# Optimization experiments

Hardware: AMD Instinct MI355X
Metric: run time of the kernel (lower is better)

## Reference

```python
import jax, jax.numpy as jnp
import numpy as np

B, T, V, C, NB, NOPS = 8, 2048, 4096, 128, 64, 8

_NONLIN = [
    lambda h: h,
    jax.nn.relu,
    lambda h: jax.nn.gelu(h, approximate=False),
    lambda h: jnp.square(h),
    lambda h: -h,
    jnp.abs,
    jnp.tanh,
    jax.nn.sigmoid,
]


def setup_inputs() -> dict:
    key = jax.random.key(0)
    ks = jax.random.split(key, 6)
    s = 0.02
    return {
        "x": jax.random.normal(ks[0], (B, T, V), dtype=jnp.float32),
        "basis": jax.random.normal(ks[1], (V, 2 * NB), dtype=jnp.float32),
        "read_coeffs": jax.random.normal(ks[2], (C, 2 * NB), dtype=jnp.float32) * s,
        "write_coeffs": jax.random.normal(ks[3], (C, 2 * NB), dtype=jnp.float32) * s,
        "op_logits": jnp.zeros((NOPS,), dtype=jnp.float32),
        "op_weights": jax.random.normal(ks[4], (NOPS, C, C), dtype=jnp.float32) * s,
        "op_biases": jnp.zeros((NOPS, C), dtype=jnp.float32),
        "out_scale": jnp.float32(0.1),
    }


def op_bank(values, op_logits, op_weights, op_biases):
    # values: (B, T, C); soft mixture of 8 small channel transforms
    w = jax.nn.softmax(op_logits)  # (n_ops,)
    result = jnp.zeros_like(values)
    for i in range(NOPS):
        h = values @ op_weights[i] + op_biases[i]
        h = _NONLIN[i % len(_NONLIN)](h)
        result = result + w[i] * h
    return result


def reference(x, basis, read_coeffs, write_coeffs, op_logits, op_weights, op_biases, out_scale):
    # READ: Fourier soft addressing over V registers, normalized over registers (axis 0)
    read_w = jax.nn.softmax(basis @ read_coeffs.T, axis=0)  # (V, C)
    values = x @ read_w  # (B, T, C)
    # SELECT OP + APPLY
    values = op_bank(values, op_logits, op_weights, op_biases)
    # WRITE: unnormalized Fourier addressing back to registers
    write_w = basis @ write_coeffs.T  # (V, C)
    return (values @ write_w.T) * out_scale  # (B, T, V)
```

## Files before the change

kernel.cpp:

```cpp
#include <hip/hip_runtime.h>
#include <math.h>

#define M_TOT 16384
#define V_DIM 4096
#define C_DIM 128

typedef __bf16 bf16;
typedef __bf16 bf16x8 __attribute__((ext_vector_type(8)));
typedef float f32x4 __attribute__((ext_vector_type(4)));

__device__ inline f32x4 zero4() { f32x4 z; z[0]=0.f; z[1]=0.f; z[2]=0.f; z[3]=0.f; return z; }

__device__ inline bf16 f2bf(float f) {
  union { float f; unsigned u; } a; a.f = f;
  unsigned r = (a.u + 0x7FFFu + ((a.u >> 16) & 1u)) >> 16;
  union { unsigned short s; bf16 b; } o; o.s = (unsigned short)r;
  return o.b;
}

__device__ inline bf16x8 cvt8(float4 a, float4 b) {
  bf16x8 r;
  r[0]=f2bf(a.x); r[1]=f2bf(a.y); r[2]=f2bf(a.z); r[3]=f2bf(a.w);
  r[4]=f2bf(b.x); r[5]=f2bf(b.y); r[6]=f2bf(b.z); r[7]=f2bf(b.w);
  return r;
}

__device__ inline void gld_lds16(const void* g, void* l) {
  __builtin_amdgcn_global_load_lds((const __attribute__((address_space(1))) void*)g,
                                   (__attribute__((address_space(3))) void*)l, 16, 0, 0);
}

union PrepU {
  struct { bf16 A[128][136]; bf16 B[128][136]; } lg;
  struct { bf16 A[64][136];  bf16 B[128][136]; } w2;
};

__global__ __launch_bounds__(256) void k_prep(const float* __restrict__ basis,
                                              const float* __restrict__ rc,
                                              const float* __restrict__ wc,
                                              const float* __restrict__ opw,
                                              float* __restrict__ LT,
                                              bf16* __restrict__ W2,
                                              bf16* __restrict__ WTO) {
  __shared__ __align__(16) PrepU pu;
  const int t = threadIdx.x;
  const int bid = blockIdx.x;
  const int lane = t & 63, wave = t >> 6, fm = lane & 15, quad = lane >> 4;

  if (bid < 32) {
    const int v0 = bid * 128;
    {
      const int row = t >> 1, c0 = (t & 1) * 64;
      const float4* p = (const float4*)(rc + row * 128 + c0);
      bf16x8* d = (bf16x8*)&pu.lg.A[row][c0];
#pragma unroll
      for (int j = 0; j < 8; j++) { float4 a = p[2*j], b = p[2*j+1]; d[j] = cvt8(a, b); }
    }
    {
      const int row = t >> 1, c0 = (t & 1) * 64;
      const float4* p = (const float4*)(basis + (size_t)(v0 + row) * 128 + c0);
      bf16x8* d = (bf16x8*)&pu.lg.B[row][c0];
#pragma unroll
      for (int j = 0; j < 8; j++) { float4 a = p[2*j], b = p[2*j+1]; d[j] = cvt8(a, b); }
    }
    __syncthreads();

    f32x4 acc[2][8];
#pragma unroll
    for (int m = 0; m < 2; m++)
#pragma unroll
      for (int n = 0; n < 8; n++) acc[m][n] = zero4();

#pragma unroll
    for (int kk = 0; kk < 4; kk++) {
      bf16x8 af[2];
#pragma unroll
      for (int m = 0; m < 2; m++)
        af[m] = *(const bf16x8*)&pu.lg.A[wave * 32 + m * 16 + fm][kk * 32 + quad * 8];
#pragma unroll
      for (int nt = 0; nt < 8; nt++) {
        bf16x8 bfr = *(const bf16x8*)&pu.lg.B[nt * 16 + fm][kk * 32 + quad * 8];
#pragma unroll
        for (int m = 0; m < 2; m++)
          acc[m][nt] = __builtin_amdgcn_mfma_f32_16x16x32_bf16(af[m], bfr, acc[m][nt], 0, 0, 0);
      }
    }
#pragma unroll
    for (int m = 0; m < 2; m++)
#pragma unroll
      for (int nt = 0; nt < 8; nt++)
#pragma unroll
        for (int r = 0; r < 4; r++) {
          int c = wave * 32 + m * 16 + quad * 4 + r;
          LT[(size_t)c * V_DIM + v0 + nt * 16 + fm] = acc[m][nt][r];
        }
  } else if (bid < 96) {
    const int v0 = (bid - 32) * 64;
    {
      const int row = t >> 2, c0 = (t & 3) * 32;
      const float4* p = (const float4*)(basis + (size_t)(v0 + row) * 128 + c0);
      bf16x8* d = (bf16x8*)&pu.w2.A[row][c0];
#pragma unroll
      for (int j = 0; j < 4; j++) { float4 a = p[2*j], b = p[2*j+1]; d[j] = cvt8(a, b); }
    }
    {
      const int row = t >> 1, c0 = (t & 1) * 64;
      const float4* p = (const float4*)(wc + row * 128 + c0);
      bf16x8* d = (bf16x8*)&pu.w2.B[row][c0];
#pragma unroll
      for (int j = 0; j < 8; j++) { float4 a = p[2*j], b = p[2*j+1]; d[j] = cvt8(a, b); }
    }
    __syncthreads();

    f32x4 acc[8];
#pragma unroll
    for (int n = 0; n < 8; n++) acc[n] = zero4();
#pragma unroll
    for (int kk = 0; kk < 4; kk++) {
      bf16x8 af = *(const bf16x8*)&pu.w2.A[wave * 16 + fm][kk * 32 + quad * 8];
#pragma unroll
      for (int nt = 0; nt < 8; nt++) {
        bf16x8 bfr = *(const bf16x8*)&pu.w2.B[nt * 16 + fm][kk * 32 + quad * 8];
        acc[nt] = __builtin_amdgcn_mfma_f32_16x16x32_bf16(af, bfr, acc[nt], 0, 0, 0);
      }
    }
#pragma unroll
    for (int nt = 0; nt < 8; nt++)
#pragma unroll
      for (int r = 0; r < 4; r++) {
        int v = v0 + wave * 16 + quad * 4 + r;
        W2[v * 128 + nt * 16 + fm] = f2bf(acc[nt][r]);
      }
  } else {
    int idx = (bid - 96) * 256 + t;
    int i = idx >> 14, rem = idx & 16383, n = rem >> 7, k = rem & 127;
    WTO[idx] = f2bf(opw[(i << 14) + k * 128 + n]);
  }
}

__global__ __launch_bounds__(256) void k_softmax(const float* __restrict__ LT,
                                                 bf16* __restrict__ RT) {
  const int c = blockIdx.x, t = threadIdx.x;
  __shared__ float red[256];
  const float* row = LT + (size_t)c * V_DIM;
  float e[16];
  float lmax = -3.0e38f;
#pragma unroll
  for (int j = 0; j < 16; j++) { e[j] = row[t + 256 * j]; lmax = fmaxf(lmax, e[j]); }
  red[t] = lmax;
  __syncthreads();
  for (int off = 128; off > 0; off >>= 1) {
    if (t < off) red[t] = fmaxf(red[t], red[t + off]);
    __syncthreads();
  }
  const float gmax = red[0];
  __syncthreads();
  float lsum = 0.f;
#pragma unroll
  for (int j = 0; j < 16; j++) { e[j] = __expf(e[j] - gmax); lsum += e[j]; }
  red[t] = lsum;
  __syncthreads();
  for (int off = 128; off > 0; off >>= 1) {
    if (t < off) red[t] += red[t + off];
    __syncthreads();
  }
  const float inv = 1.f / red[0];
#pragma unroll
  for (int j = 0; j < 16; j++)
    RT[(size_t)c * V_DIM + t + 256 * j] = f2bf(e[j] * inv);
}

__global__ __launch_bounds__(256, 4) void k_gemm1(const float* __restrict__ x,
                                                  const bf16* __restrict__ RT,
                                                  bf16* __restrict__ PART) {
  __shared__ __align__(16) bf16 Bsm[2][128][64];
  const int t = threadIdx.x;
  const int kc = blockIdx.x & 3;
  const int m0 = (blockIdx.x >> 2) * 64;
  const int lane = t & 63, wave = t >> 6;
  const int fm = lane & 15, quad = lane >> 4;
  const int sw = (fm & 7) << 4;

  const int c_row = wave * 32 + (lane >> 3);
  const int src_colbyte = ((lane & 7) * 16) ^ ((lane >> 3) << 4);
  const bf16* bp = RT + (size_t)c_row * V_DIM + (src_colbyte >> 1);

  const float* xp = x + (size_t)(m0 + wave * 16 + fm) * V_DIM + quad * 8;

  f32x4 acc[8];
#pragma unroll
  for (int i = 0; i < 8; i++) acc[i] = zero4();

  const int kbeg = kc * 1024;

#define G1_ISSUE_B(buf, koff)                                                  \
  {                                                                            \
    _Pragma("unroll")                                                          \
    for (int jj = 0; jj < 4; jj++)                                             \
      gld_lds16(bp + (size_t)jj * 8 * V_DIM + (koff),                          \
                (char*)&Bsm[buf][0][0] + (wave * 4 + jj) * 1024);              \
  }

#define G1_ISSUE_A(p0, p1, p2, p3, koff)                                       \
  {                                                                            \
    p0 = *(const float4*)(xp + (koff));                                        \
    p1 = *(const float4*)(xp + (koff) + 4);                                    \
    p2 = *(const float4*)(xp + (koff) + 32);                                   \
    p3 = *(const float4*)(xp + (koff) + 36);                                   \
  }

#define G1_COMPUTE(buf, p0, p1, p2, p3)                                        \
  {                                                                            \
    bf16x8 af0 = cvt8(p0, p1);                                                 \
    bf16x8 af1 = cvt8(p2, p3);                                                 \
    const char* bb = (const char*)&Bsm[buf][0][0];                             \
    _Pragma("unroll")                                                          \
    for (int nt = 0; nt < 8; nt++) {                                           \
      const char* rp = bb + (nt * 16 + fm) * 128;                              \
      bf16x8 b0 = *(const bf16x8*)(rp + ((quad * 16) ^ sw));                   \
      bf16x8 b1 = *(const bf16x8*)(rp + ((64 + quad * 16) ^ sw));              \
      acc[nt] = __builtin_amdgcn_mfma_f32_16x16x32_bf16(af0, b0, acc[nt], 0, 0, 0); \
      acc[nt] = __builtin_amdgcn_mfma_f32_16x16x32_bf16(af1, b1, acc[nt], 0, 0, 0); \
    }                                                                          \
  }

  float4 aE0, aE1, aE2, aE3, aO0, aO1, aO2, aO3;

  G1_ISSUE_B(0, kbeg);
  G1_ISSUE_A(aE0, aE1, aE2, aE3, kbeg);

#pragma unroll
  for (int s = 0; s < 8; s++) {
    const int k0 = kbeg + s * 128;
    __syncthreads();
    G1_ISSUE_B(1, k0 + 64);
    G1_ISSUE_A(aO0, aO1, aO2, aO3, k0 + 64);
    G1_COMPUTE(0, aE0, aE1, aE2, aE3);
    __syncthreads();
    if (s < 7) {
      G1_ISSUE_B(0, k0 + 128);
      G1_ISSUE_A(aE0, aE1, aE2, aE3, k0 + 128);
    }
    G1_COMPUTE(1, aO0, aO1, aO2, aO3);
  }
#undef G1_ISSUE_B
#undef G1_ISSUE_A
#undef G1_COMPUTE

  bf16* po = PART + (size_t)kc * (M_TOT * C_DIM);
#pragma unroll
  for (int nt = 0; nt < 8; nt++)
#pragma unroll
    for (int r = 0; r < 4; r++) {
      int row = m0 + wave * 16 + quad * 4 + r;
      po[row * 128 + nt * 16 + fm] = f2bf(acc[nt][r]);
    }
}

__device__ inline float apply_nonlin(int i, float v) {
  switch (i) {
    case 0: return v;
    case 1: return fmaxf(v, 0.f);
    case 2: return 0.5f * v * (1.f + erff(v * 0.70710678118654752f));
    case 3: return v * v;
    case 4: return -v;
    case 5: return fabsf(v);
    case 6: return tanhf(v);
    default: return 1.f / (1.f + __expf(-v));
  }
}

__global__ __launch_bounds__(256) void k_opbank(const bf16* __restrict__ PART,
                                                const bf16* __restrict__ WTO,
                                                const float* __restrict__ op_logits,
                                                const float* __restrict__ op_biases,
                                                bf16* __restrict__ val2) {
  __shared__ __align__(16) bf16 Asm[32][136];
  __shared__ __align__(16) bf16 Bsm[128][136];
  const int t = threadIdx.x;
  const int m0 = blockIdx.x * 32;
  const int lane = t & 63, wave = t >> 6;
  const int fm = lane & 15, quad = lane >> 4;
  const int mf = wave & 1, nh = wave >> 1;

  float w[8];
  {
    float lm = -3.0e38f;
#pragma unroll
    for (int i = 0; i < 8; i++) { w[i] = op_logits[i]; lm = fmaxf(lm, w[i]); }
    float s = 0.f;
#pragma unroll
    for (int i = 0; i < 8; i++) { w[i] = __expf(w[i] - lm); s += w[i]; }
    float inv = 1.f / s;
#pragma unroll
    for (int i = 0; i < 8; i++) w[i] *= inv;
  }

  {
    const int row = t >> 3, c0 = (t & 7) * 16;
    float accA[16];
#pragma unroll
    for (int j = 0; j < 16; j++) accA[j] = 0.f;
#pragma unroll
    for (int p = 0; p < 4; p++) {
      const bf16x8* q = (const bf16x8*)(PART + (size_t)p * (M_TOT * C_DIM) + (m0 + row) * 128 + c0);
      bf16x8 u0 = q[0], u1 = q[1];
#pragma unroll
      for (int j = 0; j < 8; j++) { accA[j] += (float)u0[j]; accA[8 + j] += (float)u1[j]; }
    }
    bf16x8 o0, o1;
#pragma unroll
    for (int j = 0; j < 8; j++) { o0[j] = f2bf(accA[j]); o1[j] = f2bf(accA[8 + j]); }
    *(bf16x8*)&Asm[row][c0] = o0;
    *(bf16x8*)&Asm[row][c0 + 8] = o1;
  }
  __syncthreads();

  bf16x8 af[4];
#pragma unroll
  for (int kk = 0; kk < 4; kk++)
    af[kk] = *(const bf16x8*)&Asm[mf * 16 + fm][kk * 32 + quad * 8];

  f32x4 res[4];
#pragma unroll
  for (int j = 0; j < 4; j++) res[j] = zero4();

  const int brow = t >> 1, boff = (t & 1) * 64;
  for (int i = 0; i < 8; i++) {
    __syncthreads();
    {
      const uint4* p = (const uint4*)(WTO + i * 16384 + brow * 128 + boff);
      uint4* d = (uint4*)&Bsm[brow][boff];
#pragma unroll
      for (int j = 0; j < 8; j++) d[j] = p[j];
    }
    __syncthreads();
#pragma unroll
    for (int j = 0; j < 4; j++) {
      const int nt = nh * 4 + j;
      f32x4 h = zero4();
#pragma unroll
      for (int kk = 0; kk < 4; kk++) {
        bf16x8 bfr = *(const bf16x8*)&Bsm[nt * 16 + fm][kk * 32 + quad * 8];
        h = __builtin_amdgcn_mfma_f32_16x16x32_bf16(af[kk], bfr, h, 0, 0, 0);
      }
      float bias = op_biases[i * 128 + nt * 16 + fm];
#pragma unroll
      for (int r = 0; r < 4; r++) {
        float vv = h[r] + bias;
        res[j][r] += w[i] * apply_nonlin(i, vv);
      }
    }
  }
#pragma unroll
  for (int j = 0; j < 4; j++) {
    const int nt = nh * 4 + j;
#pragma unroll
    for (int r = 0; r < 4; r++) {
      int row = m0 + mf * 16 + quad * 4 + r;
      val2[row * 128 + nt * 16 + fm] = f2bf(res[j][r]);
    }
  }
}

struct G2S { bf16 A[64][136]; bf16 B[128][136]; };
union G2U { G2S s; float C[64][132]; };

__global__ __launch_bounds__(256) void k_gemm2(const bf16* __restrict__ val2,
                                               const bf16* __restrict__ W2,
                                               const float* __restrict__ p_scale,
                                               float* __restrict__ out) {
  __shared__ __align__(16) G2U u;
  const int t = threadIdx.x;
  const int n0 = (blockIdx.x >> 8) * 128;
  const int m0 = (blockIdx.x & 255) * 64;
  const int lane = t & 63, wave = t >> 6;
  const int fm = lane & 15, quad = lane >> 4;

  {
    const int row = t >> 2, off = (t & 3) * 32;
    const uint4* p = (const uint4*)(val2 + (m0 + row) * 128 + off);
    uint4* d = (uint4*)&u.s.A[row][off];
#pragma unroll
    for (int j = 0; j < 4; j++) d[j] = p[j];
  }
  {
    const int row = t >> 1, off = (t & 1) * 64;
    const uint4* p = (const uint4*)(W2 + (n0 + row) * 128 + off);
    uint4* d = (uint4*)&u.s.B[row][off];
#pragma unroll
    for (int j = 0; j < 8; j++) d[j] = p[j];
  }
  __syncthreads();

  const float scale = *p_scale;
  bf16x8 af[4];
#pragma unroll
  for (int kk = 0; kk < 4; kk++)
    af[kk] = *(const bf16x8*)&u.s.A[wave * 16 + fm][kk * 32 + quad * 8];

  f32x4 acc[8];
#pragma unroll
  for (int nt = 0; nt < 8; nt++) {
    acc[nt] = zero4();
#pragma unroll
    for (int kk = 0; kk < 4; kk++) {
      bf16x8 bfr = *(const bf16x8*)&u.s.B[nt * 16 + fm][kk * 32 + quad * 8];
      acc[nt] = __builtin_amdgcn_mfma_f32_16x16x32_bf16(af[kk], bfr, acc[nt], 0, 0, 0);
    }
  }
  __syncthreads();
#pragma unroll
  for (int nt = 0; nt < 8; nt++)
#pragma unroll
    for (int r = 0; r < 4; r++)
      u.C[wave * 16 + quad * 4 + r][nt * 16 + fm] = acc[nt][r] * scale;
  __syncthreads();
#pragma unroll
  for (int j = 0; j < 8; j++) {
    int idx = t + 256 * j;
    int row = idx >> 5, c4 = idx & 31;
    float4 v = *(const float4*)&u.C[row][c4 * 4];
    *(float4*)(out + (size_t)(m0 + row) * V_DIM + n0 + c4 * 4) = v;
  }
}

extern "C" void kernel_launch(void* const* d_in, const int* in_sizes, int n_in,
                              void* d_out, int out_size, void* d_ws, size_t ws_size,
                              hipStream_t stream) {
  const float* x      = (const float*)d_in[0];
  const float* basis  = (const float*)d_in[1];
  const float* rc     = (const float*)d_in[2];
  const float* wc     = (const float*)d_in[3];
  const float* oplog  = (const float*)d_in[4];
  const float* opw    = (const float*)d_in[5];
  const float* opb    = (const float*)d_in[6];
  const float* oscale = (const float*)d_in[7];
  float* out = (float*)d_out;
  char* ws = (char*)d_ws;

  float* LT  = (float*)(ws);
  bf16* RT   = (bf16*)(ws + 2097152);
  bf16* W2   = (bf16*)(ws + 3145728);
  bf16* WTO  = (bf16*)(ws + 4194304);
  bf16* PART = (bf16*)(ws + 4456448);
  bf16* VAL2 = (bf16*)(ws + 21233664);

  k_prep   <<<608, 256, 0, stream>>>(basis, rc, wc, opw, LT, W2, WTO);
  k_softmax<<<C_DIM, 256, 0, stream>>>(LT, RT);
  k_gemm1  <<<(M_TOT / 64) * 4, 256, 0, stream>>>(x, RT, PART);
  k_opbank <<<M_TOT / 32, 256, 0, stream>>>(PART, WTO, oplog, opb, VAL2);
  k_gemm2  <<<(M_TOT / 64) * (V_DIM / 128), 256, 0, stream>>>(VAL2, W2, oscale, out);
}
```

Baseline: 577.3 us.

## Fuse read GEMM, op bank and write GEMM into one per-tile kernel

Replaces the split-K read GEMM, the op-bank kernel and the write GEMM with a single kernel. Each block handles 64 rows: it runs the full K=4096 reduction, then applies the eight op transforms from shared memory, then streams the output in 32 column tiles with W2 tiles prefetched through registers. The goal is to drop the partial-sum and intermediate buffers and their global round trips, plus two launches. The cost is a grid of only 256 blocks of 256 threads, so latency hiding is much weaker, and output stores now go straight from MFMA fragments instead of being staged for coalescing.

New measurement: 644.7 us. 11.7% more time.

```diff
diff --git a/kernel.cpp b/kernel.cpp
--- a/kernel.cpp
+++ b/kernel.cpp
@@ -170,93 +170,6 @@
     RT[(size_t)c * V_DIM + t + 256 * j] = f2bf(e[j] * inv);
 }
 
-__global__ __launch_bounds__(256, 4) void k_gemm1(const float* __restrict__ x,
-                                                  const bf16* __restrict__ RT,
-                                                  bf16* __restrict__ PART) {
-  __shared__ __align__(16) bf16 Bsm[2][128][64];
-  const int t = threadIdx.x;
-  const int kc = blockIdx.x & 3;
-  const int m0 = (blockIdx.x >> 2) * 64;
-  const int lane = t & 63, wave = t >> 6;
-  const int fm = lane & 15, quad = lane >> 4;
-  const int sw = (fm & 7) << 4;
-
-  const int c_row = wave * 32 + (lane >> 3);
-  const int src_colbyte = ((lane & 7) * 16) ^ ((lane >> 3) << 4);
-  const bf16* bp = RT + (size_t)c_row * V_DIM + (src_colbyte >> 1);
-
-  const float* xp = x + (size_t)(m0 + wave * 16 + fm) * V_DIM + quad * 8;
-
-  f32x4 acc[8];
-#pragma unroll
-  for (int i = 0; i < 8; i++) acc[i] = zero4();
-
-  const int kbeg = kc * 1024;
-
-#define G1_ISSUE_B(buf, koff)                                                  \
-  {                                                                            \
-    _Pragma("unroll")                                                          \
-    for (int jj = 0; jj < 4; jj++)                                             \
-      gld_lds16(bp + (size_t)jj * 8 * V_DIM + (koff),                          \
-                (char*)&Bsm[buf][0][0] + (wave * 4 + jj) * 1024);              \
-  }
-
-#define G1_ISSUE_A(p0, p1, p2, p3, koff)                                       \
-  {                                                                            \
-    p0 = *(const float4*)(xp + (koff));                                        \
-    p1 = *(const float4*)(xp + (koff) + 4);                                    \
-    p2 = *(const float4*)(xp + (koff) + 32);                                   \
-    p3 = *(const float4*)(xp + (koff) + 36);                                   \
-  }
-
-#define G1_COMPUTE(buf, p0, p1, p2, p3)                                        \
-  {                                                                            \
-    bf16x8 af0 = cvt8(p0, p1);                                                 \
-    bf16x8 af1 = cvt8(p2, p3);                                                 \
-    const char* bb = (const char*)&Bsm[buf][0][0];                             \
-    _Pragma("unroll")                                                          \
-    for (int nt = 0; nt < 8; nt++) {                                           \
-      const char* rp = bb + (nt * 16 + fm) * 128;                              \
-      bf16x8 b0 = *(const bf16x8*)(rp + ((quad * 16) ^ sw));                   \
-      bf16x8 b1 = *(const bf16x8*)(rp + ((64 + quad * 16) ^ sw));              \
-      acc[nt] = __builtin_amdgcn_mfma_f32_16x16x32_bf16(af0, b0, acc[nt], 0, 0, 0); \
-      acc[nt] = __builtin_amdgcn_mfma_f32_16x16x32_bf16(af1, b1, acc[nt], 0, 0, 0); \
-    }                                                                          \
-  }
-
-  float4 aE0, aE1, aE2, aE3, aO0, aO1, aO2, aO3;
-
-  G1_ISSUE_B(0, kbeg);
-  G1_ISSUE_A(aE0, aE1, aE2, aE3, kbeg);
-
-#pragma unroll
-  for (int s = 0; s < 8; s++) {
-    const int k0 = kbeg + s * 128;
-    __syncthreads();
-    G1_ISSUE_B(1, k0 + 64);
-    G1_ISSUE_A(aO0, aO1, aO2, aO3, k0 + 64);
-    G1_COMPUTE(0, aE0, aE1, aE2, aE3);
-    __syncthreads();
-    if (s < 7) {
-      G1_ISSUE_B(0, k0 + 128);
-      G1_ISSUE_A(aE0, aE1, aE2, aE3, k0 + 128);
-    }
-    G1_COMPUTE(1, aO0, aO1, aO2, aO3);
-  }
-#undef G1_ISSUE_B
-#undef G1_ISSUE_A
-#undef G1_COMPUTE
-
-  bf16* po = PART + (size_t)kc * (M_TOT * C_DIM);
-#pragma unroll
-  for (int nt = 0; nt < 8; nt++)
-#pragma unroll
-    for (int r = 0; r < 4; r++) {
-      int row = m0 + wave * 16 + quad * 4 + r;
-      po[row * 128 + nt * 16 + fm] = f2bf(acc[nt][r]);
-    }
-}
-
 __device__ inline float apply_nonlin(int i, float v) {
   switch (i) {
     case 0: return v;
@@ -270,158 +183,204 @@
   }
 }
 
-__global__ __launch_bounds__(256) void k_opbank(const bf16* __restrict__ PART,
-                                                const bf16* __restrict__ WTO,
-                                                const float* __restrict__ op_logits,
-                                                const float* __restrict__ op_biases,
-                                                bf16* __restrict__ val2) {
-  __shared__ __align__(16) bf16 Asm[32][136];
-  __shared__ __align__(16) bf16 Bsm[128][136];
+union MainU {
+  bf16 B2[2][128][64];
+  bf16 Bp[2][128][136];
+};
+
+__global__ __launch_bounds__(256, 1) void k_main(const float* __restrict__ x,
+                                                 const bf16* __restrict__ RT,
+                                                 const bf16* __restrict__ WTO,
+                                                 const bf16* __restrict__ W2,
+                                                 const float* __restrict__ op_logits,
+                                                 const float* __restrict__ op_biases,
+                                                 const float* __restrict__ p_scale,
+                                                 float* __restrict__ out) {
+  __shared__ __align__(16) MainU mu;
+  __shared__ __align__(16) bf16 S[64][136];
   const int t = threadIdx.x;
-  const int m0 = blockIdx.x * 32;
+  const int m0 = blockIdx.x * 64;
   const int lane = t & 63, wave = t >> 6;
   const int fm = lane & 15, quad = lane >> 4;
-  const int mf = wave & 1, nh = wave >> 1;
+  const int sw = (fm & 7) << 4;
+
+  const int c_row = wave * 32 + (lane >> 3);
+  const int src_colbyte = ((lane & 7) * 16) ^ ((lane >> 3) << 4);
+  const bf16* bp = RT + (size_t)c_row * V_DIM + (src_colbyte >> 1);
+  const float* xp = x + (size_t)(m0 + wave * 16 + fm) * V_DIM + quad * 8;
+
+  f32x4 acc[8];
+#pragma unroll
+  for (int i = 0; i < 8; i++) acc[i] = zero4();
+
+#define G1_ISSUE_B(buf, koff)                                                  \
+  {                                                                            \
+    _Pragma("unroll")                                                          \
+    for (int jj = 0; jj < 4; jj++)                                             \
+      gld_lds16(bp + (size_t)jj * 8 * V_DIM + (koff),                          \
+                (char*)&mu.B2[buf][0][0] + (wave * 4 + jj) * 1024);            \
+  }
+
+#define G1_ISSUE_A(p0, p1, p2, p3, koff)                                       \
+  {                                                                            \
+    p0 = *(const float4*)(xp + (koff));                                        \
+    p1 = *(const float4*)(xp + (koff) + 4);                                    \
+    p2 = *(const float4*)(xp + (koff) + 32);                                   \
+    p3 = *(const float4*)(xp + (koff) + 36);                                   \
+  }
+
+#define G1_COMPUTE(buf, p0, p1, p2, p3)                                        \
+  {                                                                            \
+    bf16x8 af0 = cvt8(p0, p1);                                                 \
+    bf16x8 af1 = cvt8(p2, p3);                                                 \
+    const char* bb = (const char*)&mu.B2[buf][0][0];                           \
+    _Pragma("unroll")                                                          \
+    for (int nt = 0; nt < 8; nt++) {                                           \
+      const char* rp = bb + (nt * 16 + fm) * 128;                              \
+      bf16x8 b0 = *(const bf16x8*)(rp + ((quad * 16) ^ sw));                   \
+      bf16x8 b1 = *(const bf16x8*)(rp + ((64 + quad * 16) ^ sw));              \
+      acc[nt] = __builtin_amdgcn_mfma_f32_16x16x32_bf16(af0, b0, acc[nt], 0, 0, 0); \
+      acc[nt] = __builtin_amdgcn_mfma_f32_16x16x32_bf16(af1, b1, acc[nt], 0, 0, 0); \
+    }                                                                          \
+  }
+
+  float4 aE0, aE1, aE2, aE3, aO0, aO1, aO2, aO3;
+
+  G1_ISSUE_B(0, 0);
+  G1_ISSUE_A(aE0, aE1, aE2, aE3, 0);
+
+  for (int s = 0; s < 32; s++) {
+    const int k0 = s * 128;
+    __syncthreads();
+    G1_ISSUE_B(1, k0 + 64);
+    G1_ISSUE_A(aO0, aO1, aO2, aO3, k0 + 64);
+    G1_COMPUTE(0, aE0, aE1, aE2, aE3);
+    __syncthreads();
+    if (s < 31) {
+      G1_ISSUE_B(0, k0 + 128);
+      G1_ISSUE_A(aE0, aE1, aE2, aE3, k0 + 128);
+    }
+    G1_COMPUTE(1, aO0, aO1, aO2, aO3);
+  }
+#undef G1_ISSUE_B
+#undef G1_ISSUE_A
+#undef G1_COMPUTE
+
+#pragma unroll
+  for (int nt = 0; nt < 8; nt++)
+#pragma unroll
+    for (int r = 0; r < 4; r++)
+      S[wave * 16 + quad * 4 + r][nt * 16 + fm] = f2bf(acc[nt][r]);
 
   float w[8];
   {
     float lm = -3.0e38f;
 #pragma unroll
     for (int i = 0; i < 8; i++) { w[i] = op_logits[i]; lm = fmaxf(lm, w[i]); }
-    float s = 0.f;
-#pragma unroll
-    for (int i = 0; i < 8; i++) { w[i] = __expf(w[i] - lm); s += w[i]; }
-    float inv = 1.f / s;
+    float ssum = 0.f;
+#pragma unroll
+    for (int i = 0; i < 8; i++) { w[i] = __expf(w[i] - lm); ssum += w[i]; }
+    float inv = 1.f / ssum;
 #pragma unroll
     for (int i = 0; i < 8; i++) w[i] *= inv;
   }
 
+  const int brow = t >> 1, boff = (t & 1) * 64;
+  uint4 pv[8];
   {
-    const int row = t >> 3, c0 = (t & 7) * 16;
-    float accA[16];
-#pragma unroll
-    for (int j = 0; j < 16; j++) accA[j] = 0.f;
-#pragma unroll
-    for (int p = 0; p < 4; p++) {
-      const bf16x8* q = (const bf16x8*)(PART + (size_t)p * (M_TOT * C_DIM) + (m0 + row) * 128 + c0);
-      bf16x8 u0 = q[0], u1 = q[1];
-#pragma unroll
-      for (int j = 0; j < 8; j++) { accA[j] += (float)u0[j]; accA[8 + j] += (float)u1[j]; }
-    }
-    bf16x8 o0, o1;
-#pragma unroll
-    for (int j = 0; j < 8; j++) { o0[j] = f2bf(accA[j]); o1[j] = f2bf(accA[8 + j]); }
-    *(bf16x8*)&Asm[row][c0] = o0;
-    *(bf16x8*)&Asm[row][c0 + 8] = o1;
-  }
+    const uint4* p = (const uint4*)(WTO + brow * 128 + boff);
+#pragma unroll
+    for (int j = 0; j < 8; j++) pv[j] = p[j];
+  }
+
   __syncthreads();
 
   bf16x8 af[4];
 #pragma unroll
   for (int kk = 0; kk < 4; kk++)
-    af[kk] = *(const bf16x8*)&Asm[mf * 16 + fm][kk * 32 + quad * 8];
-
-  f32x4 res[4];
-#pragma unroll
-  for (int j = 0; j < 4; j++) res[j] = zero4();
-
-  const int brow = t >> 1, boff = (t & 1) * 64;
+    af[kk] = *(const bf16x8*)&S[wave * 16 + fm][kk * 32 + quad * 8];
+
+  f32x4 res[8];
+#pragma unroll
+  for (int nt = 0; nt < 8; nt++) res[nt] = zero4();
+
+#pragma unroll
   for (int i = 0; i < 8; i++) {
-    __syncthreads();
-    {
-      const uint4* p = (const uint4*)(WTO + i * 16384 + brow * 128 + boff);
-      uint4* d = (uint4*)&Bsm[brow][boff];
-#pragma unroll
-      for (int j = 0; j < 8; j++) d[j] = p[j];
-    }
-    __syncthreads();
-#pragma unroll
-    for (int j = 0; j < 4; j++) {
-      const int nt = nh * 4 + j;
+    {
+      uint4* d = (uint4*)&mu.Bp[i & 1][brow][boff];
+#pragma unroll
+      for (int j = 0; j < 8; j++) d[j] = pv[j];
+    }
+    if (i < 7) {
+      const uint4* p = (const uint4*)(WTO + (i + 1) * 16384 + brow * 128 + boff);
+#pragma unroll
+      for (int j = 0; j < 8; j++) pv[j] = p[j];
+    }
+    __syncthreads();
+#pragma unroll
+    for (int nt = 0; nt < 8; nt++) {
       f32x4 h = zero4();
 #pragma unroll
       for (int kk = 0; kk < 4; kk++) {
-        bf16x8 bfr = *(const bf16x8*)&Bsm[nt * 16 + fm][kk * 32 + quad * 8];
+        bf16x8 bfr = *(const bf16x8*)&mu.Bp[i & 1][nt * 16 + fm][kk * 32 + quad * 8];
         h = __builtin_amdgcn_mfma_f32_16x16x32_bf16(af[kk], bfr, h, 0, 0, 0);
       }
       float bias = op_biases[i * 128 + nt * 16 + fm];
 #pragma unroll
-      for (int r = 0; r < 4; r++) {
-        float vv = h[r] + bias;
-        res[j][r] += w[i] * apply_nonlin(i, vv);
+      for (int r = 0; r < 4; r++)
+        res[nt][r] += w[i] * apply_nonlin(i, h[r] + bias);
+    }
+    __syncthreads();
+  }
+
+#pragma unroll
+  for (int nt = 0; nt < 8; nt++)
+#pragma unroll
+    for (int r = 0; r < 4; r++)
+      S[wave * 16 + quad * 4 + r][nt * 16 + fm] = f2bf(res[nt][r]);
+
+  {
+    const uint4* p = (const uint4*)(W2 + brow * 128 + boff);
+#pragma unroll
+    for (int j = 0; j < 8; j++) pv[j] = p[j];
+  }
+
+  __syncthreads();
+
+  bf16x8 af2[4];
+#pragma unroll
+  for (int kk = 0; kk < 4; kk++)
+    af2[kk] = *(const bf16x8*)&S[wave * 16 + fm][kk * 32 + quad * 8];
+
+  const float scale = *p_scale;
+
+#pragma unroll 2
+  for (int ti = 0; ti < 32; ti++) {
+    {
+      uint4* d = (uint4*)&mu.Bp[ti & 1][brow][boff];
+#pragma unroll
+      for (int j = 0; j < 8; j++) d[j] = pv[j];
+    }
+    if (ti < 31) {
+      const uint4* p = (const uint4*)(W2 + ((size_t)(ti + 1) * 128 + brow) * 128 + boff);
+#pragma unroll
+      for (int j = 0; j < 8; j++) pv[j] = p[j];
+    }
+    __syncthreads();
+#pragma unroll
+    for (int nt = 0; nt < 8; nt++) {
+      f32x4 a2 = zero4();
+#pragma unroll
+      for (int kk = 0; kk < 4; kk++) {
+        bf16x8 bfr = *(const bf16x8*)&mu.Bp[ti & 1][nt * 16 + fm][kk * 32 + quad * 8];
+        a2 = __builtin_amdgcn_mfma_f32_16x16x32_bf16(af2[kk], bfr, a2, 0, 0, 0);
       }
-    }
-  }
-#pragma unroll
-  for (int j = 0; j < 4; j++) {
-    const int nt = nh * 4 + j;
-#pragma unroll
-    for (int r = 0; r < 4; r++) {
-      int row = m0 + mf * 16 + quad * 4 + r;
-      val2[row * 128 + nt * 16 + fm] = f2bf(res[j][r]);
-    }
-  }
-}
-
-struct G2S { bf16 A[64][136]; bf16 B[128][136]; };
-union G2U { G2S s; float C[64][132]; };
-
-__global__ __launch_bounds__(256) void k_gemm2(const bf16* __restrict__ val2,
-                                               const bf16* __restrict__ W2,
-                                               const float* __restrict__ p_scale,
-                                               float* __restrict__ out) {
-  __shared__ __align__(16) G2U u;
-  const int t = threadIdx.x;
-  const int n0 = (blockIdx.x >> 8) * 128;
-  const int m0 = (blockIdx.x & 255) * 64;
-  const int lane = t & 63, wave = t >> 6;
-  const int fm = lane & 15, quad = lane >> 4;
-
-  {
-    const int row = t >> 2, off = (t & 3) * 32;
-    const uint4* p = (const uint4*)(val2 + (m0 + row) * 128 + off);
-    uint4* d = (uint4*)&u.s.A[row][off];
-#pragma unroll
-    for (int j = 0; j < 4; j++) d[j] = p[j];
-  }
-  {
-    const int row = t >> 1, off = (t & 1) * 64;
-    const uint4* p = (const uint4*)(W2 + (n0 + row) * 128 + off);
-    uint4* d = (uint4*)&u.s.B[row][off];
-#pragma unroll
-    for (int j = 0; j < 8; j++) d[j] = p[j];
-  }
-  __syncthreads();
-
-  const float scale = *p_scale;
-  bf16x8 af[4];
-#pragma unroll
-  for (int kk = 0; kk < 4; kk++)
-    af[kk] = *(const bf16x8*)&u.s.A[wave * 16 + fm][kk * 32 + quad * 8];
-
-  f32x4 acc[8];
-#pragma unroll
-  for (int nt = 0; nt < 8; nt++) {
-    acc[nt] = zero4();
-#pragma unroll
-    for (int kk = 0; kk < 4; kk++) {
-      bf16x8 bfr = *(const bf16x8*)&u.s.B[nt * 16 + fm][kk * 32 + quad * 8];
-      acc[nt] = __builtin_amdgcn_mfma_f32_16x16x32_bf16(af[kk], bfr, acc[nt], 0, 0, 0);
-    }
-  }
-  __syncthreads();
-#pragma unroll
-  for (int nt = 0; nt < 8; nt++)
-#pragma unroll
-    for (int r = 0; r < 4; r++)
-      u.C[wave * 16 + quad * 4 + r][nt * 16 + fm] = acc[nt][r] * scale;
-  __syncthreads();
-#pragma unroll
-  for (int j = 0; j < 8; j++) {
-    int idx = t + 256 * j;
-    int row = idx >> 5, c4 = idx & 31;
-    float4 v = *(const float4*)&u.C[row][c4 * 4];
-    *(float4*)(out + (size_t)(m0 + row) * V_DIM + n0 + c4 * 4) = v;
+#pragma unroll
+      for (int r = 0; r < 4; r++)
+        out[(size_t)(m0 + wave * 16 + quad * 4 + r) * V_DIM + ti * 128 + nt * 16 + fm] =
+            a2[r] * scale;
+    }
+    __syncthreads();
   }
 }
 
@@ -443,12 +402,8 @@
   bf16* RT   = (bf16*)(ws + 2097152);
   bf16* W2   = (bf16*)(ws + 3145728);
   bf16* WTO  = (bf16*)(ws + 4194304);
-  bf16* PART = (bf16*)(ws + 4456448);
-  bf16* VAL2 = (bf16*)(ws + 21233664);
 
   k_prep   <<<608, 256, 0, stream>>>(basis, rc, wc, opw, LT, W2, WTO);
   k_softmax<<<C_DIM, 256, 0, stream>>>(LT, RT);
-  k_gemm1  <<<(M_TOT / 64) * 4, 256, 0, stream>>>(x, RT, PART);
-  k_opbank <<<M_TOT / 32, 256, 0, stream>>>(PART, WTO, oplog, opb, VAL2);
-  k_gemm2  <<<(M_TOT / 64) * (V_DIM / 128), 256, 0, stream>>>(VAL2, W2, oscale, out);
-}
+  k_main   <<<M_TOT / 64, 256, 0, stream>>>(x, RT, WTO, W2, oplog, opb, oscale, out);
+}
```
